# Kernel tuning notes

Hardware: AMD Instinct MI355X
Metric: run time of the kernel (lower is better)

The kernel has to match this reference:

```python
import jax, jax.numpy as jnp
import numpy as np

B, NS, DNS, D, V, F, HID = 4096, 26, 13, 16, 100000, 128, 1024
N = NS + DNS  # 39 total fields for CIN
EPS = 1e-5


def setup_inputs() -> dict:
    key = jax.random.key(0)
    ks = jax.random.split(key, 32)
    s = 0.05
    d1, d2, d3 = HID, HID // 2, HID // 4
    din = NS * D + DNS  # 429
    return {
        'dense_x': jax.random.normal(ks[0], (B, DNS), jnp.float32),
        'discrete_x': jax.random.randint(ks[1], (B, NS), 0, V, jnp.int32),
        'lin_emb': jax.random.normal(ks[2], (NS, V, 1), jnp.float32) * s,
        'emb_W': jax.random.normal(ks[3], (NS, V, D), jnp.float32) * s,
        'dense_W': jax.random.normal(ks[4], (DNS, 1), jnp.float32) * s,
        'dense_b': jnp.zeros((1,), jnp.float32),
        'W1': jax.random.normal(ks[5], (din, d1), jnp.float32) * s,
        'b1': jnp.zeros((d1,), jnp.float32),
        'bn1_g': jnp.ones((d1,), jnp.float32),
        'bn1_b': jnp.zeros((d1,), jnp.float32),
        'W2': jax.random.normal(ks[6], (d1, d2), jnp.float32) * s,
        'b2': jnp.zeros((d2,), jnp.float32),
        'bn2_g': jnp.ones((d2,), jnp.float32),
        'bn2_b': jnp.zeros((d2,), jnp.float32),
        'W3': jax.random.normal(ks[7], (d2, d3), jnp.float32) * s,
        'b3': jnp.zeros((d3,), jnp.float32),
        'bn3_g': jnp.ones((d3,), jnp.float32),
        'bn3_b': jnp.zeros((d3,), jnp.float32),
        'Wout': jax.random.normal(ks[8], (d3, 1), jnp.float32) * s,
        'bout': jnp.zeros((1,), jnp.float32),
        'dense_proj': jax.random.normal(ks[9], (DNS, D), jnp.float32) * s,
        'cin_W0': jax.random.normal(ks[10], (F, N, N), jnp.float32) * s,
        'cin_W1': jax.random.normal(ks[11], (F, F, N), jnp.float32) * s,
        'cin_W2': jax.random.normal(ks[12], (F, F, N), jnp.float32) * s,
        'cin_out_W': jax.random.normal(ks[13], (3 * F, 1), jnp.float32) * s,
        'cin_out_b': jnp.zeros((1,), jnp.float32),
    }


def _bn_eval(x, g, b):
    # BatchNorm1d in eval mode with default running stats (mean=0, var=1)
    return x * (g / jnp.sqrt(1.0 + EPS)) + b


def reference(dense_x, discrete_x, lin_emb, emb_W, dense_W, dense_b,
              W1, b1, bn1_g, bn1_b, W2, b2, bn2_g, bn2_b, W3, b3, bn3_g, bn3_b,
              Wout, bout, dense_proj, cin_W0, cin_W1, cin_W2, cin_out_W, cin_out_b):
    fld = jnp.arange(NS)
    # linear part
    linear_logits = dense_x @ dense_W + dense_b + lin_emb[fld, discrete_x].sum(axis=1)  # [B,1]
    # embeddings: [B, NS, D]
    x_embeds = emb_W[fld, discrete_x]
    # DNN part
    h = jnp.concatenate([x_embeds.reshape(x_embeds.shape[0], -1), dense_x], axis=1)
    h = jax.nn.relu(_bn_eval(h @ W1 + b1, bn1_g, bn1_b))
    h = jax.nn.relu(_bn_eval(h @ W2 + b2, bn2_g, bn2_b))
    h = jax.nn.relu(_bn_eval(h @ W3 + b3, bn3_g, bn3_b))
    dnn_logits = h @ Wout + bout  # [B,1]
    # CIN part: x0 = [B, N, D] with dense features projected to embed space
    x0 = jnp.concatenate([x_embeds, dense_x[:, :, None] * dense_proj], axis=1)
    xj = x0
    p_list = []
    for W in (cin_W0, cin_W1, cin_W2):
        # hadamard[b,c,n,d] = xj[b,c,d] * x0[b,n,d]; contract with W[f,c,n], sum over c,n
        cin_out = jnp.einsum('bcd,bnd,fcn->bfd', xj, x0, W)  # [B,F,D]
        p_list.append(cin_out.sum(axis=-1))  # [B,F]
        xj = cin_out
    cin_logits = jnp.concatenate(p_list, axis=1) @ cin_out_W + cin_out_b  # [B,1]
    return linear_logits + dnn_logits + cin_logits
```

## Files before the change

kernel.cpp:

```cpp
#include <hip/hip_runtime.h>

typedef unsigned short u16;
typedef unsigned int u32;
typedef __attribute__((ext_vector_type(8))) short bf16x8;
typedef __attribute__((ext_vector_type(4))) float f32x4;

#define BB 4096
#define NS 26
#define DNS 13
#define DD 16
#define VV 100000
#define FF 128
#define NF 39
#define BD 65536
#define DIN_PAD 448

__device__ __forceinline__ float bf2f(u16 x) {
    union { u32 u; float f; } v; v.u = ((u32)x) << 16; return v.f;
}
__device__ __forceinline__ u16 f2bf(float f) {
    union { float f; u32 u; } v; v.f = f;
    u32 u = v.u;
    u32 r = (u + 0x7fffu + ((u >> 16) & 1u)) >> 16;
    return (u16)r;
}


__global__ void prep_x0_k(const float* __restrict__ emb_W, const int* __restrict__ disc,
                          const float* __restrict__ dense_x, const float* __restrict__ dense_proj,
                          u16* __restrict__ x0) {
    int e = blockIdx.x * 256 + threadIdx.x;
    int c = e & 63;
    int j = e >> 6;
    int b = j >> 4, d = j & 15;
    float v = 0.f;
    if (c < NS) {
        int ix = disc[b * NS + c];
        v = emb_W[((size_t)c * VV + ix) * DD + d];
    } else if (c < NF) {
        int q = c - NS;
        v = dense_x[b * DNS + q] * dense_proj[q * DD + d];
    }
    x0[e] = f2bf(v);
}

__global__ void prep_h0_k(const float* __restrict__ emb_W, const int* __restrict__ disc,
                          const float* __restrict__ dense_x, u16* __restrict__ h0) {
    int e = blockIdx.x * 256 + threadIdx.x;
    int col = e % DIN_PAD;
    int b = e / DIN_PAD;
    float v = 0.f;
    if (col < NS * DD) {
        int n = col >> 4, d = col & 15;
        int ix = disc[b * NS + n];
        v = emb_W[((size_t)n * VV + ix) * DD + d];
    } else if (col < NS * DD + DNS) {
        v = dense_x[b * DNS + col - NS * DD];
    }
    h0[e] = f2bf(v);
}

__global__ void transpose_pad_k(const float* __restrict__ src, u16* __restrict__ dst,
                                int K, int Nn, int Kpad) {
    int e = blockIdx.x * 256 + threadIdx.x;
    int n = e / Kpad, k = e % Kpad;
    dst[e] = (k < K) ? f2bf(src[(size_t)k * Nn + n]) : (u16)0;
}

__global__ void cinw_k(const float* __restrict__ src, u16* __restrict__ dst, int C, int Cpad) {
    int e = blockIdx.x * 256 + threadIdx.x;
    int n = e / (128 * Cpad);
    int rem = e % (128 * Cpad);
    int f = rem / Cpad, c = rem % Cpad;
    dst[e] = (c < C) ? f2bf(src[((size_t)f * C + c) * NF + n]) : (u16)0;
}

__global__ __launch_bounds__(256) void gemm_bn_relu_k(
    const u16* __restrict__ A, const u16* __restrict__ Bt, u16* __restrict__ C,
    int M, int N, int K,
    const float* __restrict__ bias, const float* __restrict__ g, const float* __restrict__ bb)
{
    __shared__ u16 la[64 * 40];
    __shared__ u16 lb[64 * 40];
    const int tid = threadIdx.x;
    const int lane = tid & 63, wave = tid >> 6;
    const int quad = lane >> 4, l16 = lane & 15;
    const int m0 = blockIdx.y * 64, n0 = blockIdx.x * 64;
    const f32x4 fzero = {0.f, 0.f, 0.f, 0.f};
    f32x4 acc[4];
    #pragma unroll
    for (int t = 0; t < 4; ++t) acc[t] = fzero;
    const int r = tid >> 2, cc = (tid & 3) * 8;
    for (int k0 = 0; k0 < K; k0 += 32) {
        __syncthreads();
        *(int4*)&la[r * 40 + cc] = *(const int4*)&A[(size_t)(m0 + r) * K + k0 + cc];
        *(int4*)&lb[r * 40 + cc] = *(const int4*)&Bt[(size_t)(n0 + r) * K + k0 + cc];
        __syncthreads();
        bf16x8 af = *(const bf16x8*)&la[(wave * 16 + l16) * 40 + quad * 8];
        #pragma unroll
        for (int t = 0; t < 4; ++t) {
            bf16x8 bfm = *(const bf16x8*)&lb[(t * 16 + l16) * 40 + quad * 8];
            acc[t] = __builtin_amdgcn_mfma_f32_16x16x32_bf16(af, bfm, acc[t], 0, 0, 0);
        }
    }
    const float rs = rsqrtf(1.f + 1e-5f);
    #pragma unroll
    for (int t = 0; t < 4; ++t) {
        int n = n0 + t * 16 + l16;
        float bi = bias[n];
        float sc = g[n] * rs;
        float b2 = bb[n];
        #pragma unroll
        for (int rr = 0; rr < 4; ++rr) {
            int m = m0 + wave * 16 + quad * 4 + rr;
            float v = (acc[t][rr] + bi) * sc + b2;
            v = fmaxf(v, 0.f);
            C[(size_t)m * N + n] = f2bf(v);
        }
    }
}

#define LOADA(buf, n_) do { \
    _Pragma("unroll") for (int ms = 0; ms < 2; ++ms) \
    _Pragma("unroll") for (int kc = 0; kc < NCH; ++kc) \
        buf[ms][kc] = *(const bf16x8*)(ap[ms][kc] + (size_t)(n_) * WSTRIDE); \
} while (0)

#define LOADX(xv, n_) do { \
    _Pragma("unroll") for (int js = 0; js < 4; ++js) \
        xv[js] = bf2f(lx0[(jh * 64 + js * 16 + l16) * 72 + (n_)]); \
} while (0)

#define COMPUTE(A, xv) do { \
    _Pragma("unroll") for (int js = 0; js < 4; ++js) { \
        f32x4 s0 = fzero, s1 = fzero; \
        _Pragma("unroll") for (int kc = 0; kc < NCH; ++kc) { \
            s0 = __builtin_amdgcn_mfma_f32_16x16x32_bf16(A[0][kc], bfr[js][kc], s0, 0, 0, 0); \
            s1 = __builtin_amdgcn_mfma_f32_16x16x32_bf16(A[1][kc], bfr[js][kc], s1, 0, 0, 0); \
        } \
        acc[js][0] += xv[js] * s0; \
        acc[js][1] += xv[js] * s1; \
    } \
} while (0)

template <int CPAD>
__global__ __launch_bounds__(512, 2) void cin_layer_k(
    const u16* __restrict__ Xj, const u16* __restrict__ X0w,
    const u16* __restrict__ Wr, u16* __restrict__ Out)
{
    constexpr int NCH = CPAD / 32;
    constexpr size_t WSTRIDE = (size_t)128 * CPAD;
    __shared__ u16 lx0[128 * 72];
    const int tid = threadIdx.x;
    const int lane = tid & 63, wave = tid >> 6;
    const int quad = lane >> 4, l16 = lane & 15;
    const int fw = wave & 3;
    const int jh = wave >> 2;
    const size_t j0 = (size_t)blockIdx.x * 128;
    const f32x4 fzero = {0.f, 0.f, 0.f, 0.f};

    for (int ch = tid; ch < 128 * 8; ch += 512) {
        int r = ch >> 3, c = (ch & 7) * 8;
        *(int4*)&lx0[r * 72 + c] = *(const int4*)&X0w[(j0 + r) * 64 + c];
    }

    bf16x8 bfr[4][NCH];
    #pragma unroll
    for (int js = 0; js < 4; ++js)
        #pragma unroll
        for (int kc = 0; kc < NCH; ++kc)
            bfr[js][kc] = *(const bf16x8*)&Xj[(j0 + jh * 64 + js * 16 + l16) * CPAD + kc * 32 + quad * 8];

    const u16* ap[2][NCH];
    #pragma unroll
    for (int ms = 0; ms < 2; ++ms)
        #pragma unroll
        for (int kc = 0; kc < NCH; ++kc)
            ap[ms][kc] = &Wr[(size_t)(fw * 32 + ms * 16 + l16) * CPAD + kc * 32 + quad * 8];

    __syncthreads();

    f32x4 acc[4][2];
    #pragma unroll
    for (int js = 0; js < 4; ++js) { acc[js][0] = fzero; acc[js][1] = fzero; }

    bf16x8 a0[2][NCH], a1[2][NCH];
    float xv0[4], xv1[4];
    LOADA(a0, 0); LOADX(xv0, 0);
    #pragma unroll 1
    for (int n = 0; n < NF - 1; n += 2) {
        LOADA(a1, n + 1); LOADX(xv1, n + 1);
        COMPUTE(a0, xv0);
        LOADA(a0, n + 2); LOADX(xv0, n + 2);
        COMPUTE(a1, xv1);
    }
    COMPUTE(a0, xv0);

    #pragma unroll
    for (int js = 0; js < 4; ++js) {
        size_t jrow = j0 + jh * 64 + js * 16 + l16;
        #pragma unroll
        for (int ms = 0; ms < 2; ++ms) {
            f32x4 v = acc[js][ms];
            uint2 pk;
            pk.x = (u32)f2bf(v[0]) | ((u32)f2bf(v[1]) << 16);
            pk.y = (u32)f2bf(v[2]) | ((u32)f2bf(v[3]) << 16);
            *(uint2*)&Out[jrow * 128 + fw * 32 + ms * 16 + quad * 4] = pk;
        }
    }
}
#undef LOADA
#undef LOADX
#undef COMPUTE

__global__ __launch_bounds__(64) void final_k(
    const float* __restrict__ dense_x, const int* __restrict__ disc,
    const float* __restrict__ lin_emb, const float* __restrict__ dense_W,
    const float* __restrict__ dense_b, const u16* __restrict__ h3,
    const float* __restrict__ Wout, const float* __restrict__ bout,
    const u16* __restrict__ out0, const u16* __restrict__ out1, const u16* __restrict__ out2,
    const float* __restrict__ cw, const float* __restrict__ cb, float* __restrict__ out)
{
    const int b = blockIdx.x;
    const int lane = threadIdx.x;
    float t = 0.f;
    if (lane < DNS) {
        t += dense_x[b * DNS + lane] * dense_W[lane];
    } else if (lane < DNS + NS) {
        int i = lane - DNS;
        t += lin_emb[(size_t)i * VV + disc[b * NS + i]];
    }
    const u16* hr = h3 + (size_t)b * 256;
    #pragma unroll
    for (int rr = 0; rr < 4; ++rr) {
        int c = lane * 4 + rr;
        t += bf2f(hr[c]) * Wout[c];
    }
    const u16* obs[3] = {out0, out1, out2};
    #pragma unroll
    for (int L = 0; L < 3; ++L) {
        const u16* ob = obs[L] + (size_t)b * 16 * 128;
        #pragma unroll
        for (int h = 0; h < 2; ++h) {
            int f = lane + h * 64;
            float p = 0.f;
            #pragma unroll
            for (int d = 0; d < 16; ++d) p += bf2f(ob[d * 128 + f]);
            t += p * cw[L * 128 + f];
        }
    }
    #pragma unroll
    for (int off = 32; off > 0; off >>= 1) t += __shfl_down(t, off, 64);
    if (lane == 0) out[b] = t + dense_b[0] + bout[0] + cb[0];
}

extern "C" void kernel_launch(void* const* d_in, const int* in_sizes, int n_in,
                              void* d_out, int out_size, void* d_ws, size_t ws_size,
                              hipStream_t stream) {
    const float* dense_x = (const float*)d_in[0];
    const int* disc      = (const int*)d_in[1];
    const float* lin_emb = (const float*)d_in[2];
    const float* emb_W   = (const float*)d_in[3];
    const float* dense_W = (const float*)d_in[4];
    const float* dense_b = (const float*)d_in[5];
    const float* W1  = (const float*)d_in[6];
    const float* b1  = (const float*)d_in[7];
    const float* g1  = (const float*)d_in[8];
    const float* bb1 = (const float*)d_in[9];
    const float* W2  = (const float*)d_in[10];
    const float* b2  = (const float*)d_in[11];
    const float* g2  = (const float*)d_in[12];
    const float* bb2 = (const float*)d_in[13];
    const float* W3  = (const float*)d_in[14];
    const float* b3  = (const float*)d_in[15];
    const float* g3  = (const float*)d_in[16];
    const float* bb3 = (const float*)d_in[17];
    const float* Wout = (const float*)d_in[18];
    const float* bout = (const float*)d_in[19];
    const float* dense_proj = (const float*)d_in[20];
    const float* cin_W0 = (const float*)d_in[21];
    const float* cin_W1 = (const float*)d_in[22];
    const float* cin_W2 = (const float*)d_in[23];
    const float* cin_ow = (const float*)d_in[24];
    const float* cin_ob = (const float*)d_in[25];

    u16* p = (u16*)d_ws;
    u16* x0  = p; p += (size_t)BD * 64;
    u16* h0  = p; p += (size_t)BB * DIN_PAD;
    u16* h1  = p; p += (size_t)BB * 1024;
    u16* h2  = p; p += (size_t)BB * 512;
    u16* h3  = p; p += (size_t)BB * 256;
    u16* W1t = p; p += (size_t)1024 * DIN_PAD;
    u16* W2t = p; p += (size_t)512 * 1024;
    u16* W3t = p; p += (size_t)256 * 512;
    u16* W0r = p; p += (size_t)NF * 128 * 64;
    u16* W1r = p; p += (size_t)NF * 128 * 128;
    u16* W2r = p; p += (size_t)NF * 128 * 128;
    u16* o0  = p; p += (size_t)BD * 128;
    u16* o1  = p; p += (size_t)BD * 128;
    u16* o2  = p; p += (size_t)BD * 128;

    prep_x0_k<<<BD * 64 / 256, 256, 0, stream>>>(emb_W, disc, dense_x, dense_proj, x0);
    prep_h0_k<<<BB * DIN_PAD / 256, 256, 0, stream>>>(emb_W, disc, dense_x, h0);
    transpose_pad_k<<<1024 * DIN_PAD / 256, 256, 0, stream>>>(W1, W1t, 429, 1024, DIN_PAD);
    transpose_pad_k<<<512 * 1024 / 256, 256, 0, stream>>>(W2, W2t, 1024, 512, 1024);
    transpose_pad_k<<<256 * 512 / 256, 256, 0, stream>>>(W3, W3t, 512, 256, 512);
    cinw_k<<<NF * 128 * 64 / 256, 256, 0, stream>>>(cin_W0, W0r, 39, 64);
    cinw_k<<<NF * 128 * 128 / 256, 256, 0, stream>>>(cin_W1, W1r, 128, 128);
    cinw_k<<<NF * 128 * 128 / 256, 256, 0, stream>>>(cin_W2, W2r, 128, 128);

    gemm_bn_relu_k<<<dim3(1024 / 64, BB / 64), 256, 0, stream>>>(h0, W1t, h1, BB, 1024, DIN_PAD, b1, g1, bb1);
    gemm_bn_relu_k<<<dim3(512 / 64, BB / 64), 256, 0, stream>>>(h1, W2t, h2, BB, 512, 1024, b2, g2, bb2);
    gemm_bn_relu_k<<<dim3(256 / 64, BB / 64), 256, 0, stream>>>(h2, W3t, h3, BB, 256, 512, b3, g3, bb3);

    cin_layer_k<64><<<BD / 128, 512, 0, stream>>>(x0, x0, W0r, o0);
    cin_layer_k<128><<<BD / 128, 512, 0, stream>>>(o0, x0, W1r, o1);
    cin_layer_k<128><<<BD / 128, 512, 0, stream>>>(o1, x0, W2r, o2);

    final_k<<<BB, 64, 0, stream>>>(dense_x, disc, lin_emb, dense_W, dense_b,
                                   h3, Wout, bout, o0, o1, o2, cin_ow, cin_ob, (float*)d_out);
}
```

Before: 723.3 us.

## Restructure CIN layer tiling and use shared-memory tiled weight transposes

```diff
diff --git a/kernel.cpp b/kernel.cpp
--- a/kernel.cpp
+++ b/kernel.cpp
@@ -62,17 +62,42 @@
 
 __global__ void transpose_pad_k(const float* __restrict__ src, u16* __restrict__ dst,
                                 int K, int Nn, int Kpad) {
-    int e = blockIdx.x * 256 + threadIdx.x;
-    int n = e / Kpad, k = e % Kpad;
-    dst[e] = (k < K) ? f2bf(src[(size_t)k * Nn + n]) : (u16)0;
+    __shared__ u16 t[64][72];
+    const int kb = blockIdx.x * 64, nb = blockIdx.y * 64;
+    for (int i = threadIdx.x; i < 64 * 64; i += 256) {
+        int kk = i >> 6, nn = i & 63;
+        int k = kb + kk, n = nb + nn;
+        float v = (k < K && n < Nn) ? src[(size_t)k * Nn + n] : 0.f;
+        t[nn][kk] = f2bf(v);
+    }
+    __syncthreads();
+    for (int i = threadIdx.x; i < 64 * 64; i += 256) {
+        int nn = i >> 6, kk = i & 63;
+        int n = nb + nn, k = kb + kk;
+        if (n < Nn && k < Kpad) dst[(size_t)n * Kpad + k] = t[nn][kk];
+    }
 }
 
 __global__ void cinw_k(const float* __restrict__ src, u16* __restrict__ dst, int C, int Cpad) {
-    int e = blockIdx.x * 256 + threadIdx.x;
-    int n = e / (128 * Cpad);
-    int rem = e % (128 * Cpad);
-    int f = rem / Cpad, c = rem % Cpad;
-    dst[e] = (c < C) ? f2bf(src[((size_t)f * C + c) * NF + n]) : (u16)0;
+    __shared__ u16 tile[256][40];
+    const int fc0 = blockIdx.x * 256;
+    const int total = 128 * C;
+    for (int i = threadIdx.x; i < 256 * NF; i += 256) {
+        int e = fc0 * NF + i;
+        if (e < total * NF) {
+            int fcl = i / NF, n = i % NF;
+            tile[fcl][n] = f2bf(src[e]);
+        }
+    }
+    __syncthreads();
+    for (int i = threadIdx.x; i < 256 * NF; i += 256) {
+        int n = i >> 8, fcl = i & 255;
+        int fc = fc0 + fcl;
+        if (fc < total) {
+            int f = fc / C, c = fc % C;
+            dst[(size_t)n * 128 * Cpad + f * Cpad + c] = tile[fcl][n];
+        }
+    }
 }
 
 __global__ __launch_bounds__(256) void gemm_bn_relu_k(
@@ -121,62 +146,54 @@
 }
 
 #define LOADA(buf, n_) do { \
+    const u16* _p = awp + (size_t)(n_) * WSTRIDE; \
     _Pragma("unroll") for (int ms = 0; ms < 2; ++ms) \
     _Pragma("unroll") for (int kc = 0; kc < NCH; ++kc) \
-        buf[ms][kc] = *(const bf16x8*)(ap[ms][kc] + (size_t)(n_) * WSTRIDE); \
+        buf[ms][kc] = *(const bf16x8*)(_p + ms * 16 * CPAD + kc * 32); \
 } while (0)
 
-#define LOADX(xv, n_) do { \
-    _Pragma("unroll") for (int js = 0; js < 4; ++js) \
-        xv[js] = bf2f(lx0[(jh * 64 + js * 16 + l16) * 72 + (n_)]); \
-} while (0)
-
-#define COMPUTE(A, xv) do { \
+#define COMPUTE(A, n_) do { \
     _Pragma("unroll") for (int js = 0; js < 4; ++js) { \
+        int jr = js * 16 + l16; \
         f32x4 s0 = fzero, s1 = fzero; \
         _Pragma("unroll") for (int kc = 0; kc < NCH; ++kc) { \
-            s0 = __builtin_amdgcn_mfma_f32_16x16x32_bf16(A[0][kc], bfr[js][kc], s0, 0, 0, 0); \
-            s1 = __builtin_amdgcn_mfma_f32_16x16x32_bf16(A[1][kc], bfr[js][kc], s1, 0, 0, 0); \
+            bf16x8 bfr = *(const bf16x8*)&lxj[jr * LDB + kc * 32 + quad * 8]; \
+            s0 = __builtin_amdgcn_mfma_f32_16x16x32_bf16(A[0][kc], bfr, s0, 0, 0, 0); \
+            s1 = __builtin_amdgcn_mfma_f32_16x16x32_bf16(A[1][kc], bfr, s1, 0, 0, 0); \
         } \
-        acc[js][0] += xv[js] * s0; \
-        acc[js][1] += xv[js] * s1; \
+        float xv = bf2f(lx0[jr * 72 + (n_)]); \
+        acc[js][0] += xv * s0; \
+        acc[js][1] += xv * s1; \
     } \
 } while (0)
 
 template <int CPAD>
-__global__ __launch_bounds__(512, 2) void cin_layer_k(
+__global__ __launch_bounds__(256, 3) void cin_layer_k(
     const u16* __restrict__ Xj, const u16* __restrict__ X0w,
     const u16* __restrict__ Wr, u16* __restrict__ Out)
 {
     constexpr int NCH = CPAD / 32;
+    constexpr int LDB = CPAD + 8;
     constexpr size_t WSTRIDE = (size_t)128 * CPAD;
-    __shared__ u16 lx0[128 * 72];
+    __shared__ u16 lxj[64 * LDB];
+    __shared__ u16 lx0[64 * 72];
     const int tid = threadIdx.x;
     const int lane = tid & 63, wave = tid >> 6;
     const int quad = lane >> 4, l16 = lane & 15;
-    const int fw = wave & 3;
-    const int jh = wave >> 2;
-    const size_t j0 = (size_t)blockIdx.x * 128;
+    const size_t j0 = (size_t)blockIdx.x * 64;
     const f32x4 fzero = {0.f, 0.f, 0.f, 0.f};
 
-    for (int ch = tid; ch < 128 * 8; ch += 512) {
+    constexpr int CHR = CPAD / 8;
+    for (int ch = tid; ch < 64 * CHR; ch += 256) {
+        int r = ch / CHR, c = (ch % CHR) * 8;
+        *(int4*)&lxj[r * LDB + c] = *(const int4*)&Xj[(j0 + r) * CPAD + c];
+    }
+    for (int ch = tid; ch < 64 * 8; ch += 256) {
         int r = ch >> 3, c = (ch & 7) * 8;
         *(int4*)&lx0[r * 72 + c] = *(const int4*)&X0w[(j0 + r) * 64 + c];
     }
 
-    bf16x8 bfr[4][NCH];
-    #pragma unroll
-    for (int js = 0; js < 4; ++js)
-        #pragma unroll
-        for (int kc = 0; kc < NCH; ++kc)
-            bfr[js][kc] = *(const bf16x8*)&Xj[(j0 + jh * 64 + js * 16 + l16) * CPAD + kc * 32 + quad * 8];
-
-    const u16* ap[2][NCH];
-    #pragma unroll
-    for (int ms = 0; ms < 2; ++ms)
-        #pragma unroll
-        for (int kc = 0; kc < NCH; ++kc)
-            ap[ms][kc] = &Wr[(size_t)(fw * 32 + ms * 16 + l16) * CPAD + kc * 32 + quad * 8];
+    const u16* awp = Wr + (size_t)(wave * 32 + l16) * CPAD + quad * 8;
 
     __syncthreads();
 
@@ -185,32 +202,30 @@
     for (int js = 0; js < 4; ++js) { acc[js][0] = fzero; acc[js][1] = fzero; }
 
     bf16x8 a0[2][NCH], a1[2][NCH];
-    float xv0[4], xv1[4];
-    LOADA(a0, 0); LOADX(xv0, 0);
+    LOADA(a0, 0);
     #pragma unroll 1
     for (int n = 0; n < NF - 1; n += 2) {
-        LOADA(a1, n + 1); LOADX(xv1, n + 1);
-        COMPUTE(a0, xv0);
-        LOADA(a0, n + 2); LOADX(xv0, n + 2);
-        COMPUTE(a1, xv1);
-    }
-    COMPUTE(a0, xv0);
+        LOADA(a1, n + 1);
+        COMPUTE(a0, n);
+        LOADA(a0, n + 2);
+        COMPUTE(a1, n + 1);
+    }
+    COMPUTE(a0, NF - 1);
 
     #pragma unroll
     for (int js = 0; js < 4; ++js) {
-        size_t jrow = j0 + jh * 64 + js * 16 + l16;
+        size_t jrow = j0 + js * 16 + l16;
         #pragma unroll
         for (int ms = 0; ms < 2; ++ms) {
             f32x4 v = acc[js][ms];
             uint2 pk;
             pk.x = (u32)f2bf(v[0]) | ((u32)f2bf(v[1]) << 16);
             pk.y = (u32)f2bf(v[2]) | ((u32)f2bf(v[3]) << 16);
-            *(uint2*)&Out[jrow * 128 + fw * 32 + ms * 16 + quad * 4] = pk;
+            *(uint2*)&Out[jrow * 128 + wave * 32 + ms * 16 + quad * 4] = pk;
         }
     }
 }
 #undef LOADA
-#undef LOADX
 #undef COMPUTE
 
 __global__ __launch_bounds__(64) void final_k(
@@ -302,20 +317,21 @@
 
     prep_x0_k<<<BD * 64 / 256, 256, 0, stream>>>(emb_W, disc, dense_x, dense_proj, x0);
     prep_h0_k<<<BB * DIN_PAD / 256, 256, 0, stream>>>(emb_W, disc, dense_x, h0);
-    transpose_pad_k<<<1024 * DIN_PAD / 256, 256, 0, stream>>>(W1, W1t, 429, 1024, DIN_PAD);
-    transpose_pad_k<<<512 * 1024 / 256, 256, 0, stream>>>(W2, W2t, 1024, 512, 1024);
-    transpose_pad_k<<<256 * 512 / 256, 256, 0, stream>>>(W3, W3t, 512, 256, 512);
-    cinw_k<<<NF * 128 * 64 / 256, 256, 0, stream>>>(cin_W0, W0r, 39, 64);
-    cinw_k<<<NF * 128 * 128 / 256, 256, 0, stream>>>(cin_W1, W1r, 128, 128);
-    cinw_k<<<NF * 128 * 128 / 256, 256, 0, stream>>>(cin_W2, W2r, 128, 128);
+    transpose_pad_k<<<dim3(DIN_PAD / 64, 1024 / 64), 256, 0, stream>>>(W1, W1t, 429, 1024, DIN_PAD);
+    transpose_pad_k<<<dim3(1024 / 64, 512 / 64), 256, 0, stream>>>(W2, W2t, 1024, 512, 1024);
+    transpose_pad_k<<<dim3(512 / 64, 256 / 64), 256, 0, stream>>>(W3, W3t, 512, 256, 512);
+    hipMemsetAsync(W0r, 0, (size_t)NF * 128 * 64 * sizeof(u16), stream);
+    cinw_k<<<(128 * 39 + 255) / 256, 256, 0, stream>>>(cin_W0, W0r, 39, 64);
+    cinw_k<<<128 * 128 / 256, 256, 0, stream>>>(cin_W1, W1r, 128, 128);
+    cinw_k<<<128 * 128 / 256, 256, 0, stream>>>(cin_W2, W2r, 128, 128);
 
     gemm_bn_relu_k<<<dim3(1024 / 64, BB / 64), 256, 0, stream>>>(h0, W1t, h1, BB, 1024, DIN_PAD, b1, g1, bb1);
     gemm_bn_relu_k<<<dim3(512 / 64, BB / 64), 256, 0, stream>>>(h1, W2t, h2, BB, 512, 1024, b2, g2, bb2);
     gemm_bn_relu_k<<<dim3(256 / 64, BB / 64), 256, 0, stream>>>(h2, W3t, h3, BB, 256, 512, b3, g3, bb3);
 
-    cin_layer_k<64><<<BD / 128, 512, 0, stream>>>(x0, x0, W0r, o0);
-    cin_layer_k<128><<<BD / 128, 512, 0, stream>>>(o0, x0, W1r, o1);
-    cin_layer_k<128><<<BD / 128, 512, 0, stream>>>(o1, x0, W2r, o2);
+    cin_layer_k<64><<<BD / 64, 256, 0, stream>>>(x0, x0, W0r, o0);
+    cin_layer_k<128><<<BD / 64, 256, 0, stream>>>(o0, x0, W1r, o1);
+    cin_layer_k<128><<<BD / 64, 256, 0, stream>>>(o1, x0, W2r, o2);
 
     final_k<<<BB, 64, 0, stream>>>(dense_x, disc, lin_emb, dense_W, dense_b,
                                    h3, Wout, bout, o0, o1, o2, cin_ow, cin_ob, (float*)d_out);
```

Measured after the change: 907.4 us. 25.4% more time.
